# Kernel tuning notes

Hardware: AMD Instinct MI355X
Metric: run time of the kernel (lower is better)

Reference implementation:

```python
import jax, jax.numpy as jnp
import numpy as np

B, D_IN = 8192, 1024
E, T = 8, 4
H1, H2, H3 = 1024, 512, 256


def setup_inputs() -> dict:
    key = jax.random.key(0)
    ks = jax.random.split(key, 8)
    s1 = 1.0 / np.sqrt(D_IN)
    s2 = 1.0 / np.sqrt(H1)
    s3 = 1.0 / np.sqrt(H2)
    return {
        "x": jax.random.normal(ks[0], (B, D_IN), jnp.float32),
        "W1": jax.random.normal(ks[1], (E, D_IN, H1), jnp.float32) * s1,
        "b1": jnp.zeros((E, H1), jnp.float32),
        "W2": jax.random.normal(ks[2], (E, H1, H2), jnp.float32) * s2,
        "b2": jnp.zeros((E, H2), jnp.float32),
        "W3": jax.random.normal(ks[3], (E, H2, H3), jnp.float32) * s3,
        "b3": jnp.zeros((E, H3), jnp.float32),
        "gate_w": jax.random.normal(ks[4], (D_IN, T * E), jnp.float32) * 0.05,
    }


def reference(x, W1, b1, W2, b2, W3, b3, gate_w):
    # Expert MLPs, vectorized over experts: h = relu(x @ W + b)
    h = jax.nn.relu(jnp.einsum("bi,eio->beo", x, W1) + b1[None])      # [B,E,H1]
    h = jax.nn.relu(jnp.einsum("beh,eho->beo", h, W2) + b2[None])     # [B,E,H2]
    h = jax.nn.relu(jnp.einsum("beh,eho->beo", h, W3) + b3[None])     # [B,E,H3]
    expert_outputs = jnp.transpose(h, (0, 2, 1))                       # [B,D_out,E]

    # Gates: logits [B, T*E] -> [B,T,E], softmax over experts, -> [B,E,T]
    logits = (x @ gate_w).reshape(B, T, E)
    gates = jax.nn.softmax(logits, axis=2)
    gates = jnp.transpose(gates, (0, 2, 1))                            # [B,E,T]

    mmoe_output = jnp.matmul(expert_outputs, gates)                    # [B,D_out,T]
    # unstack along task axis -> tuple of T [B, D_out] arrays
    return tuple(mmoe_output[:, :, t] for t in range(T))
```

## Files before the change

kernel.cpp:

```cpp
#include <hip/hip_runtime.h>


#define B_ROWS 8192
#define D_IN   1024
#define NEXP   8
#define NTASK  4
#define H1     1024
#define H2     512
#define H3     256

typedef __attribute__((ext_vector_type(8))) short bf16x8;
typedef __attribute__((ext_vector_type(4))) float f32x4;

__device__ __forceinline__ unsigned short f2bf(float f) {
    union { float f; unsigned int u; } x; x.f = f;
    unsigned int r = x.u + 0x7fffu + ((x.u >> 16) & 1u);
    return (unsigned short)(r >> 16);
}
__device__ __forceinline__ float bf2f(unsigned short u) {
    union { unsigned int u; float f; } x; x.u = ((unsigned int)u) << 16;
    return x.f;
}

__device__ __forceinline__ void gload_lds16(const void* gptr, void* lptr) {
    __builtin_amdgcn_global_load_lds(
        (__attribute__((address_space(1))) void*)gptr,
        (__attribute__((address_space(3))) void*)lptr,
        16, 0, 0);
}

struct __align__(8) us4 { unsigned short x, y, z, w; };

__global__ void convert_x_kernel(const float* __restrict__ x,
                                 unsigned short* __restrict__ xb) {
    int i = blockIdx.x * blockDim.x + threadIdx.x;
    float4 v = ((const float4*)x)[i];
    us4 o;
    o.x = f2bf(v.x); o.y = f2bf(v.y); o.z = f2bf(v.z); o.w = f2bf(v.w);
    ((us4*)xb)[i] = o;
}

__global__ void transpose_convert_kernel(const float* __restrict__ W,
                                         unsigned short* __restrict__ Wt,
                                         int K, int N) {
    __shared__ float tile[32][33];
    const int e = blockIdx.z;
    const float* We = W + (size_t)e * K * N;
    unsigned short* Wte = Wt + (size_t)e * K * N;
    const int k0 = blockIdx.x * 32, n0 = blockIdx.y * 32;
    const int tx = threadIdx.x, ty = threadIdx.y;
#pragma unroll
    for (int i = 0; i < 4; ++i)
        tile[ty + i * 8][tx] = We[(size_t)(k0 + ty + i * 8) * N + n0 + tx];
    __syncthreads();
#pragma unroll
    for (int i = 0; i < 4; ++i)
        Wte[(size_t)(n0 + ty + i * 8) * K + k0 + tx] = f2bf(tile[tx][ty + i * 8]);
}

__global__ __launch_bounds__(256) void gemm_bias_relu_kernel(
    const unsigned short* __restrict__ A, long long Aes,
    const unsigned short* __restrict__ Bt, long long Bes,
    const float* __restrict__ bias, long long bias_es,
    unsigned short* __restrict__ C, long long Ces,
    int M, int N, int K) {
    __shared__ __align__(16) unsigned short sA[128 * 64];
    __shared__ __align__(16) unsigned short sB[128 * 64];

    const int tid  = threadIdx.x;
    const int lane = tid & 63;
    const int w    = tid >> 6;
    const int wr   = w >> 1, wc = w & 1;
    const int quad = lane >> 4, l15 = lane & 15;
    const int r8   = lane >> 3;
    const int c8   = lane & 7;
    const int gchunk = c8 ^ r8;

    const int e  = blockIdx.z;
    const int m0 = blockIdx.x * 128;
    const int n0 = blockIdx.y * 128;

    A    += (size_t)e * Aes;
    Bt   += (size_t)e * Bes;
    bias += (size_t)e * bias_es;
    C    += (size_t)e * Ces;

    f32x4 acc[4][4] = {};

    const int swz = (l15 & 7);

    for (int k0 = 0; k0 < K; k0 += 64) {
#pragma unroll
        for (int q = 0; q < 4; ++q) {
            const int row = w * 32 + q * 8 + r8;
            gload_lds16(A + (size_t)(m0 + row) * K + k0 + gchunk * 8,
                        &sA[row * 64 + c8 * 8]);
        }
#pragma unroll
        for (int q = 0; q < 4; ++q) {
            const int row = w * 32 + q * 8 + r8;
            gload_lds16(Bt + (size_t)(n0 + row) * K + k0 + gchunk * 8,
                        &sB[row * 64 + c8 * 8]);
        }
        __syncthreads();

#pragma unroll
        for (int s = 0; s < 2; ++s) {
            const int cs = ((s * 4 + quad) ^ swz) * 8;
            bf16x8 af[4], bfv[4];
#pragma unroll
            for (int i = 0; i < 4; ++i)
                af[i] = *(const bf16x8*)&sA[(wr * 64 + i * 16 + l15) * 64 + cs];
#pragma unroll
            for (int j = 0; j < 4; ++j)
                bfv[j] = *(const bf16x8*)&sB[(wc * 64 + j * 16 + l15) * 64 + cs];
#pragma unroll
            for (int i = 0; i < 4; ++i)
#pragma unroll
                for (int j = 0; j < 4; ++j)
                    acc[i][j] = __builtin_amdgcn_mfma_f32_16x16x32_bf16(
                        af[i], bfv[j], acc[i][j], 0, 0, 0);
        }
        __syncthreads();
    }

#pragma unroll
    for (int j = 0; j < 4; ++j) {
        const int col = n0 + wc * 64 + j * 16 + l15;
        const float bv = bias[col];
#pragma unroll
        for (int i = 0; i < 4; ++i) {
#pragma unroll
            for (int r = 0; r < 4; ++r) {
                const int row = m0 + wr * 64 + i * 16 + quad * 4 + r;
                float v = acc[i][j][r] + bv;
                v = v > 0.f ? v : 0.f;
                C[(size_t)row * N + col] = f2bf(v);
            }
        }
    }
}

__global__ void gates_kernel(const float* __restrict__ x,
                             const float* __restrict__ gw,
                             float* __restrict__ gates) {
    const int tid = threadIdx.x;
    const int o = tid & 31;
    const int r = tid >> 5;
    const int b = blockIdx.x * 8 + r;
    const float* xr = x + (size_t)b * D_IN;
    float acc = 0.f;
    for (int k = 0; k < D_IN; k += 4) {
        float4 xv = *(const float4*)&xr[k];
        acc += xv.x * gw[(k + 0) * 32 + o];
        acc += xv.y * gw[(k + 1) * 32 + o];
        acc += xv.z * gw[(k + 2) * 32 + o];
        acc += xv.w * gw[(k + 3) * 32 + o];
    }
    float m = acc;
    m = fmaxf(m, __shfl_xor(m, 1));
    m = fmaxf(m, __shfl_xor(m, 2));
    m = fmaxf(m, __shfl_xor(m, 4));
    float ex = __expf(acc - m);
    float s = ex;
    s += __shfl_xor(s, 1);
    s += __shfl_xor(s, 2);
    s += __shfl_xor(s, 4);
    gates[(size_t)b * 32 + o] = ex / s;
}

__global__ void combine_kernel(const unsigned short* __restrict__ h3,
                               const float* __restrict__ gates,
                               float* __restrict__ out) {
    __shared__ float g[32];
    const int b = blockIdx.x;
    const int d = threadIdx.x;
    if (d < 32) g[d] = gates[(size_t)b * 32 + d];
    __syncthreads();
    float acc[NTASK] = {0.f, 0.f, 0.f, 0.f};
#pragma unroll
    for (int e = 0; e < NEXP; ++e) {
        const float h = bf2f(h3[((size_t)e * B_ROWS + b) * H3 + d]);
#pragma unroll
        for (int t = 0; t < NTASK; ++t) acc[t] += h * g[t * 8 + e];
    }
#pragma unroll
    for (int t = 0; t < NTASK; ++t)
        out[((size_t)t * B_ROWS + b) * H3 + d] = acc[t];
}

#define OFF_XBF 0u
#define OFF_W1T 16777216u
#define OFF_W2T 33554432u
#define OFF_W3T 41943040u
#define OFF_G   44040192u
#define OFF_H1  45088768u
#define OFF_H2  179306496u
#define OFF_H3  45088768u

extern "C" void kernel_launch(void* const* d_in, const int* in_sizes, int n_in,
                              void* d_out, int out_size, void* d_ws, size_t ws_size,
                              hipStream_t stream) {
    const float* x  = (const float*)d_in[0];
    const float* W1 = (const float*)d_in[1];
    const float* b1 = (const float*)d_in[2];
    const float* W2 = (const float*)d_in[3];
    const float* b2 = (const float*)d_in[4];
    const float* W3 = (const float*)d_in[5];
    const float* b3 = (const float*)d_in[6];
    const float* gw = (const float*)d_in[7];
    float* out = (float*)d_out;
    char* ws = (char*)d_ws;

    unsigned short* xbf = (unsigned short*)(ws + OFF_XBF);
    unsigned short* w1t = (unsigned short*)(ws + OFF_W1T);
    unsigned short* w2t = (unsigned short*)(ws + OFF_W2T);
    unsigned short* w3t = (unsigned short*)(ws + OFF_W3T);
    float*          gts = (float*)(ws + OFF_G);
    unsigned short* h1  = (unsigned short*)(ws + OFF_H1);
    unsigned short* h2  = (unsigned short*)(ws + OFF_H2);
    unsigned short* h3  = (unsigned short*)(ws + OFF_H3);

    convert_x_kernel<<<dim3((B_ROWS * D_IN) / 4 / 256), dim3(256), 0, stream>>>(x, xbf);
    transpose_convert_kernel<<<dim3(D_IN / 32, H1 / 32, NEXP), dim3(32, 8), 0, stream>>>(W1, w1t, D_IN, H1);
    transpose_convert_kernel<<<dim3(H1 / 32, H2 / 32, NEXP), dim3(32, 8), 0, stream>>>(W2, w2t, H1, H2);
    transpose_convert_kernel<<<dim3(H2 / 32, H3 / 32, NEXP), dim3(32, 8), 0, stream>>>(W3, w3t, H2, H3);

    gates_kernel<<<dim3(B_ROWS / 8), dim3(256), 0, stream>>>(x, gw, gts);

    gemm_bias_relu_kernel<<<dim3(B_ROWS / 128, H1 / 128, NEXP), dim3(256), 0, stream>>>(
        xbf, 0LL,
        w1t, (long long)H1 * D_IN,
        b1, (long long)H1,
        h1, (long long)B_ROWS * H1,
        B_ROWS, H1, D_IN);
    gemm_bias_relu_kernel<<<dim3(B_ROWS / 128, H2 / 128, NEXP), dim3(256), 0, stream>>>(
        h1, (long long)B_ROWS * H1,
        w2t, (long long)H2 * H1,
        b2, (long long)H2,
        h2, (long long)B_ROWS * H2,
        B_ROWS, H2, H1);
    gemm_bias_relu_kernel<<<dim3(B_ROWS / 128, H3 / 128, NEXP), dim3(256), 0, stream>>>(
        h2, (long long)B_ROWS * H2,
        w3t, (long long)H3 * H2,
        b3, (long long)H3,
        h3, (long long)B_ROWS * H3,
        B_ROWS, H3, H2);

    combine_kernel<<<dim3(B_ROWS), dim3(256), 0, stream>>>(h3, gts, out);
}
```

Baseline: 501.8 us.

## Double-buffer LDS tiles in expert GEMM to overlap global loads with MFMA

Restructures the GEMM main loop to use two LDS buffers for the A and B tiles. The next K-tile is prefetched via global_load_lds while MFMAs consume the current one, which leaves one barrier per iteration instead of two. Base pointers are hoisted out of the loop, and launch bounds now request two blocks per CU. The cost is double the LDS footprint (64KB per block), which can limit occupancy.

```diff
diff --git a/kernel.cpp b/kernel.cpp
--- a/kernel.cpp
+++ b/kernel.cpp
@@ -58,14 +58,14 @@
         Wte[(size_t)(n0 + ty + i * 8) * K + k0 + tx] = f2bf(tile[tx][ty + i * 8]);
 }
 
-__global__ __launch_bounds__(256) void gemm_bias_relu_kernel(
+__global__ __launch_bounds__(256, 2) void gemm_bias_relu_kernel(
     const unsigned short* __restrict__ A, long long Aes,
     const unsigned short* __restrict__ Bt, long long Bes,
     const float* __restrict__ bias, long long bias_es,
     unsigned short* __restrict__ C, long long Ces,
     int M, int N, int K) {
-    __shared__ __align__(16) unsigned short sA[128 * 64];
-    __shared__ __align__(16) unsigned short sB[128 * 64];
+    __shared__ __align__(16) unsigned short sA[2][128 * 64];
+    __shared__ __align__(16) unsigned short sB[2][128 * 64];
 
     const int tid  = threadIdx.x;
     const int lane = tid & 63;
@@ -89,31 +89,44 @@
 
     const int swz = (l15 & 7);
 
-    for (int k0 = 0; k0 < K; k0 += 64) {
-#pragma unroll
-        for (int q = 0; q < 4; ++q) {
-            const int row = w * 32 + q * 8 + r8;
-            gload_lds16(A + (size_t)(m0 + row) * K + k0 + gchunk * 8,
-                        &sA[row * 64 + c8 * 8]);
+    const unsigned short* Abase = A + (size_t)(m0 + w * 32 + r8) * K + gchunk * 8;
+    const unsigned short* Bbase = Bt + (size_t)(n0 + w * 32 + r8) * K + gchunk * 8;
+    unsigned short* sAw = &sA[0][(w * 32 + r8) * 64 + c8 * 8];
+    unsigned short* sBw = &sB[0][(w * 32 + r8) * 64 + c8 * 8];
+
+    const int niter = K >> 6;
+
+#pragma unroll
+    for (int q = 0; q < 4; ++q) {
+        gload_lds16(Abase + (size_t)(q * 8) * K, sAw + q * 8 * 64);
+        gload_lds16(Bbase + (size_t)(q * 8) * K, sBw + q * 8 * 64);
+    }
+
+    for (int it = 0; it < niter; ++it) {
+        __syncthreads();
+        if (it + 1 < niter) {
+            const int buf = (it + 1) & 1;
+            const size_t koff = (size_t)(it + 1) << 6;
+#pragma unroll
+            for (int q = 0; q < 4; ++q) {
+                gload_lds16(Abase + (size_t)(q * 8) * K + koff,
+                            sAw + buf * (128 * 64) + q * 8 * 64);
+                gload_lds16(Bbase + (size_t)(q * 8) * K + koff,
+                            sBw + buf * (128 * 64) + q * 8 * 64);
+            }
         }
-#pragma unroll
-        for (int q = 0; q < 4; ++q) {
-            const int row = w * 32 + q * 8 + r8;
-            gload_lds16(Bt + (size_t)(n0 + row) * K + k0 + gchunk * 8,
-                        &sB[row * 64 + c8 * 8]);
-        }
-        __syncthreads();
-
+        const unsigned short* a_ = sA[it & 1];
+        const unsigned short* b_ = sB[it & 1];
 #pragma unroll
         for (int s = 0; s < 2; ++s) {
             const int cs = ((s * 4 + quad) ^ swz) * 8;
             bf16x8 af[4], bfv[4];
 #pragma unroll
             for (int i = 0; i < 4; ++i)
-                af[i] = *(const bf16x8*)&sA[(wr * 64 + i * 16 + l15) * 64 + cs];
+                af[i] = *(const bf16x8*)&a_[(wr * 64 + i * 16 + l15) * 64 + cs];
 #pragma unroll
             for (int j = 0; j < 4; ++j)
-                bfv[j] = *(const bf16x8*)&sB[(wc * 64 + j * 16 + l15) * 64 + cs];
+                bfv[j] = *(const bf16x8*)&b_[(wc * 64 + j * 16 + l15) * 64 + cs];
 #pragma unroll
             for (int i = 0; i < 4; ++i)
 #pragma unroll
@@ -121,7 +134,6 @@
                     acc[i][j] = __builtin_amdgcn_mfma_f32_16x16x32_bf16(
                         af[i], bfv[j], acc[i][j], 0, 0, 0);
         }
-        __syncthreads();
     }
 
 #pragma unroll
```

New measurement: 490.0 us. 1.02x faster.
